# Performance work log

Hardware: AMD Instinct MI355X
Metric: run time of the kernel (lower is better)

The kernel has to match this reference:

```python
import jax, jax.numpy as jnp
import numpy as np

H = 1024   # hidden_dim
NH = 16    # num_heads
HD = H // NH  # head_dim = 64
B, S = 2, 2048
LN_EPS = 1e-5


def setup_inputs() -> dict:
    key = jax.random.key(0)
    ks = jax.random.split(key, 5)
    scale = 1.0 / np.sqrt(H)  # xavier-ish scale for stability
    return {
        "x": jax.random.normal(ks[0], (B, S, H), dtype=jnp.float32),
        "Wq": jax.random.normal(ks[1], (H, H), dtype=jnp.float32) * scale,
        "bq": jnp.zeros((H,), jnp.float32),
        "Wk": jax.random.normal(ks[2], (H, H), dtype=jnp.float32) * scale,
        "bk": jnp.zeros((H,), jnp.float32),
        "Wv": jax.random.normal(ks[3], (H, H), dtype=jnp.float32) * scale,
        "bv": jnp.zeros((H,), jnp.float32),
        "Wo": jax.random.normal(ks[4], (H, H), dtype=jnp.float32) * scale,
        "bo": jnp.zeros((H,), jnp.float32),
        "ln_gamma": jnp.ones((H,), jnp.float32),
        "ln_beta": jnp.zeros((H,), jnp.float32),
    }


def reference(x, Wq, bq, Wk, bk, Wv, bv, Wo, bo, ln_gamma, ln_beta):
    b, s, _ = x.shape
    # QKV projections, split heads: (b, nh, s, hd)
    def split_heads(t):
        return t.reshape(b, s, NH, HD).transpose(0, 2, 1, 3)
    Q = split_heads(x @ Wq + bq)
    K = split_heads(x @ Wk + bk)
    V = split_heads(x @ Wv + bv)
    # scaled dot-product with clamp (mask=None path)
    scores = jnp.einsum('bhqd,bhkd->bhqk', Q, K) / np.sqrt(HD).astype(np.float32)
    scores = jnp.clip(scores, -10000.0, 10000.0)
    attn = jax.nn.softmax(scores, axis=-1)
    # dropout is identity in eval mode
    ctx = jnp.einsum('bhqk,bhkd->bhqd', attn, V)
    ctx = ctx.transpose(0, 2, 1, 3).reshape(b, s, H)
    out = ctx @ Wo + bo
    # residual + LayerNorm
    y = out + x
    mu = jnp.mean(y, axis=-1, keepdims=True)
    var = jnp.mean(jnp.square(y - mu), axis=-1, keepdims=True)
    y = (y - mu) * jax.lax.rsqrt(var + LN_EPS)
    return y * ln_gamma + ln_beta
```

## Files before the change

### kernel.cpp

```cpp
#include <hip/hip_runtime.h>

typedef unsigned short u16;
typedef __attribute__((ext_vector_type(8))) short shortx8;
typedef __attribute__((ext_vector_type(4))) float floatx4;
typedef __attribute__((ext_vector_type(2))) float floatx2;
typedef __attribute__((ext_vector_type(2))) unsigned uintx2;
typedef __attribute__((ext_vector_type(4))) unsigned uintx4;

#define GLD16(gp, lp) __builtin_amdgcn_global_load_lds( \
    (__attribute__((address_space(1))) void*)(gp), \
    (__attribute__((address_space(3))) void*)(lp), 16, 0, 0)

#define BAR() __builtin_amdgcn_s_barrier()
#define LGKM0() do { asm volatile("s_waitcnt lgkmcnt(0)" ::: "memory"); \
                     __builtin_amdgcn_sched_barrier(0); } while (0)
#define VMCNT0() do { asm volatile("s_waitcnt vmcnt(0)" ::: "memory"); \
                      __builtin_amdgcn_sched_barrier(0); } while (0)

__device__ __forceinline__ u16 f2bf(float f) {
  union { float f; unsigned u; } v; v.f = f;
  unsigned r = v.u + 0x7FFFu + ((v.u >> 16) & 1u);
  return (u16)(r >> 16);
}

__device__ __forceinline__ unsigned pkbf(float a, float b) {
#if __has_builtin(__builtin_amdgcn_cvt_pk_bf16_f32)
  auto r = __builtin_amdgcn_cvt_pk_bf16_f32(a, b);
  return __builtin_bit_cast(unsigned, r);
#else
  union { float f; unsigned u; } x, y; x.f = a; y.f = b;
  return __builtin_amdgcn_perm(y.u + 0x8000u, x.u + 0x8000u, 0x07060302u);
#endif
}

__global__ __launch_bounds__(256) void prep_kernel(const float* __restrict__ x,
                                                   u16* __restrict__ xb,
                                                   const float* __restrict__ Wq,
                                                   const float* __restrict__ Wk,
                                                   const float* __restrict__ Wv,
                                                   const float* __restrict__ Wo,
                                                   u16* __restrict__ Wt) {
  __shared__ u16 tile[32][33];
  int bid = blockIdx.x;
  int tid = threadIdx.x;
  if (bid < 4096) {
    int i = bid * 256 + tid;
    float4 v = ((const float4*)x)[i];
    uintx2 o;
    o.x = pkbf(v.x, v.y);
    o.y = pkbf(v.z, v.w);
    ((uintx2*)xb)[i] = o;
  } else {
    int block = bid - 4096;
    int mat = block >> 10;
    int rem = block & 1023;
    const float* W = (mat == 0) ? Wq : (mat == 1) ? Wk : (mat == 2) ? Wv : Wo;
    u16* dst = Wt + (size_t)mat * 1024 * 1024;
    int n0 = (rem & 31) * 32, k0 = (rem >> 5) * 32;
    int tx = tid & 31, ty = tid >> 5;
    for (int i = 0; i < 4; ++i)
      tile[ty + i * 8][tx] = f2bf(W[(size_t)(k0 + ty + i * 8) * 1024 + n0 + tx]);
    __syncthreads();
    for (int i = 0; i < 4; ++i)
      dst[(size_t)(n0 + ty + i * 8) * 1024 + k0 + tx] = tile[tx][ty + i * 8];
  }
}

template <int MIB>
__device__ __forceinline__ void qkv_lda(const u16* Ah, int lrow, int lcol,
                                        shortx8 (&afr)[2][2]) {
#pragma unroll
  for (int j = 0; j < 2; ++j) {
    int rm = (MIB + j) * 16 + lcol;
#pragma unroll
    for (int kk = 0; kk < 2; ++kk)
      afr[j][kk] = *(const shortx8*)&Ah[rm * 64 + (((kk * 4 + lrow) ^ (rm & 7)) * 8)];
  }
}

template <int MIB>
__device__ __forceinline__ void qkv_mfma(floatx4 (&acc)[8][4],
                                         const shortx8 (&afr)[2][2],
                                         const shortx8 (&bfr)[4][2]) {
#pragma unroll
  for (int kk = 0; kk < 2; ++kk)
#pragma unroll
    for (int j = 0; j < 2; ++j)
#pragma unroll
      for (int ni = 0; ni < 4; ++ni)
        acc[MIB + j][ni] = __builtin_amdgcn_mfma_f32_16x16x32_bf16(
            afr[j][kk], bfr[ni][kk], acc[MIB + j][ni], 0, 0, 0);
}

__global__ __launch_bounds__(512, 2) void qkv_gemm(const u16* __restrict__ xb,
                                                   const u16* __restrict__ Wt,
                                                   const float* __restrict__ bq,
                                                   const float* __restrict__ bk,
                                                   const float* __restrict__ bv,
                                                   u16* __restrict__ Qh,
                                                   u16* __restrict__ Kh,
                                                   u16* __restrict__ Vth) {
  __shared__ u16 lds[65536];
  const int tid = threadIdx.x;
  const int wave = tid >> 6, lane = tid & 63;
  const int lrow = lane >> 4, lcol = lane & 15;
  const int wm = wave >> 2, wn = wave & 3;
  const int m0 = blockIdx.x * 256;
  const int nt = blockIdx.y;
  const int mat = nt >> 2;
  const int n0 = (nt & 3) * 256;
  const u16* Ag = xb;
  const u16* Bg = Wt + (size_t)mat * 1048576;

  const u16* sa[2][2];
  const u16* sb[2][2];
#pragma unroll
  for (int h = 0; h < 2; ++h)
#pragma unroll
    for (int l = 0; l < 2; ++l) {
      int g = (l * 8 + wave) * 64 + lane;
      int r = g >> 3, c = g & 7;
      int cc = (c ^ (r & 7)) * 8;
      sa[h][l] = Ag + (size_t)(m0 + h * 128 + r) * 1024 + cc;
      sb[h][l] = Bg + (size_t)(n0 + h * 128 + r) * 1024 + cc;
    }

  floatx4 acc[8][4];
#pragma unroll
  for (int mi = 0; mi < 8; ++mi)
#pragma unroll
    for (int ni = 0; ni < 4; ++ni)
      acc[mi][ni] = (floatx4){0.f, 0.f, 0.f, 0.f};

#pragma unroll
  for (int h = 0; h < 2; ++h)
#pragma unroll
    for (int l = 0; l < 2; ++l) {
      GLD16(sa[h][l], lds + h * 8192 + (l * 8 + wave) * 512);
      GLD16(sb[h][l], lds + 16384 + h * 8192 + (l * 8 + wave) * 512);
    }
  VMCNT0();
  BAR();

#pragma unroll 2
  for (int t = 0; t < 16; ++t) {
    const int rb = t & 1, wb = rb ^ 1;
    const u16* Ah = lds + rb * 32768 + wm * 8192;
    const u16* Bh = lds + rb * 32768 + 16384 + (wn >> 1) * 8192;
    u16* Aw = lds + wb * 32768;
    u16* Bw = lds + wb * 32768 + 16384;

    if (t < 15) {
      int k64 = (t + 1) * 64;
#pragma unroll
      for (int l = 0; l < 2; ++l) {
        GLD16(sa[0][l] + k64, Aw + (l * 8 + wave) * 512);
        GLD16(sa[1][l] + k64, Aw + 8192 + (l * 8 + wave) * 512);
      }
    }
    shortx8 bfr[4][2];
#pragma unroll
    for (int ni = 0; ni < 4; ++ni) {
      int rn = (wn & 1) * 64 + ni * 16 + lcol;
#pragma unroll
      for (int kk = 0; kk < 2; ++kk)
        bfr[ni][kk] = *(const shortx8*)&Bh[rn * 64 + (((kk * 4 + lrow) ^ (rn & 7)) * 8)];
    }
    {
      shortx8 afr[2][2];
      qkv_lda<0>(Ah, lrow, lcol, afr);
      BAR();
      LGKM0();
      __builtin_amdgcn_s_setprio(1);
      qkv_mfma<0>(acc, afr, bfr);
      __builtin_amdgcn_s_setprio(0);
      BAR();
    }
    if (t < 15) {
      int k64 = (t + 1) * 64;
#pragma unroll
      for (int l = 0; l < 2; ++l) {
        GLD16(sb[0][l] + k64, Bw + (l * 8 + wave) * 512);
        GLD16(sb[1][l] + k64, Bw + 8192 + (l * 8 + wave) * 512);
      }
    }
    {
      shortx8 afr[2][2];
      qkv_lda<2>(Ah, lrow, lcol, afr);
      BAR();
      LGKM0();
      __builtin_amdgcn_s_setprio(1);
      qkv_mfma<2>(acc, afr, bfr);
      __builtin_amdgcn_s_setprio(0);
      BAR();
    }
    {
      shortx8 afr[2][2];
      qkv_lda<4>(Ah, lrow, lcol, afr);
      BAR();
      LGKM0();
      __builtin_amdgcn_s_setprio(1);
      qkv_mfma<4>(acc, afr, bfr);
      __builtin_amdgcn_s_setprio(0);
      BAR();
    }
    {
      shortx8 afr[2][2];
      qkv_lda<6>(Ah, lrow, lcol, afr);
      BAR();
      LGKM0();
      __builtin_amdgcn_s_setprio(1);
      qkv_mfma<6>(acc, afr, bfr);
      __builtin_amdgcn_s_setprio(0);
      VMCNT0();
      BAR();
    }
  }

  const float* bias = (mat == 0) ? bq : (mat == 1) ? bk : bv;
  const float qscale = 0.18033688011f;

  if (mat < 2) {
    u16* dst = (mat == 0) ? Qh : Kh;
    float sc = (mat == 0) ? qscale : 1.0f;
#pragma unroll
    for (int mi = 0; mi < 8; ++mi) {
      int mb = wm * 128 + mi * 16 + lrow * 4;
#pragma unroll
      for (int ni = 0; ni < 4; ++ni) {
        int n = wn * 64 + ni * 16 + lcol;
        float bval = bias[n0 + n];
#pragma unroll
        for (int r = 0; r < 4; ++r) {
          int m = mb + r;
          lds[m * 256 + (((n >> 3) ^ (m & 31)) * 8) + (n & 7)] =
              f2bf((acc[mi][ni][r] + bval) * sc);
        }
      }
    }
    __syncthreads();
    int row = tid >> 1, half = tid & 1;
    int m = m0 + row;
    int bb = m >> 11, s = m & 2047;
#pragma unroll
    for (int i = 0; i < 16; ++i) {
      int cg = half * 16 + i;
      int pg = cg ^ (row & 31);
      shortx8 v = *(const shortx8*)&lds[row * 256 + pg * 8];
      int ng = n0 + cg * 8;
      int hh = ng >> 6, d = ng & 63;
      *(shortx8*)&dst[((size_t)(bb * 16 + hh) * 2048 + s) * 64 + d] = v;
    }
  } else {
#pragma unroll
    for (int mi = 0; mi < 8; ++mi) {
      int mbase = m0 + wm * 128 + mi * 16 + lrow * 4;
      int bb = mbase >> 11, s = mbase & 2047;
#pragma unroll
      for (int ni = 0; ni < 4; ++ni) {
        int n = n0 + wn * 64 + ni * 16 + lcol;
        float bval = bias[n];
        int hh = n >> 6, d = n & 63;
        uintx2 pk;
        pk.x = pkbf(acc[mi][ni][0] + bval, acc[mi][ni][1] + bval);
        pk.y = pkbf(acc[mi][ni][2] + bval, acc[mi][ni][3] + bval);
        *(uintx2*)&Vth[((size_t)(bb * 16 + hh) * 64 + d) * 2048 + s] = pk;
      }
    }
  }
}

__global__ __launch_bounds__(256, 2) void out_gemm(const u16* __restrict__ ctx,
                                                   const u16* __restrict__ Wot,
                                                   const float* __restrict__ bo,
                                                   float* __restrict__ aout) {
  __shared__ u16 lds[24576];
  const int tid = threadIdx.x;
  const int wave = tid >> 6, lane = tid & 63;
  const int lrow = lane >> 4, lcol = lane & 15;
  const int wm = wave >> 1, wn = wave & 1;
  const int m0 = blockIdx.x * 128;
  const int n0 = blockIdx.y * 64;

  const u16* sa[4];
  const u16* sb[2];
#pragma unroll
  for (int l = 0; l < 4; ++l) {
    int g = (l * 4 + wave) * 64 + lane;
    int r = g >> 3, c = g & 7;
    sa[l] = ctx + (size_t)(m0 + r) * 1024 + ((c ^ (r & 7)) * 8);
  }
#pragma unroll
  for (int l = 0; l < 2; ++l) {
    int g = (l * 4 + wave) * 64 + lane;
    int r = g >> 3, c = g & 7;
    sb[l] = Wot + (size_t)(n0 + r) * 1024 + ((c ^ (r & 7)) * 8);
  }

  floatx4 acc[4][2];
#pragma unroll
  for (int mi = 0; mi < 4; ++mi)
#pragma unroll
    for (int ni = 0; ni < 2; ++ni)
      acc[mi][ni] = (floatx4){0.f, 0.f, 0.f, 0.f};

#pragma unroll
  for (int l = 0; l < 4; ++l) GLD16(sa[l], lds + (l * 4 + wave) * 512);
#pragma unroll
  for (int l = 0; l < 2; ++l) GLD16(sb[l], lds + 8192 + (l * 4 + wave) * 512);
  VMCNT0();
  BAR();

#pragma unroll 2
  for (int t = 0; t < 16; ++t) {
    const int rb = t & 1, wb = rb ^ 1;
    const u16* Ab = lds + rb * 12288;
    const u16* Bb = lds + rb * 12288 + 8192;
    u16* Aw = lds + wb * 12288;
    u16* Bw = lds + wb * 12288 + 8192;
    const int k64 = (t + 1) * 64;

    if (t < 15) {
#pragma unroll
      for (int l = 0; l < 4; ++l) GLD16(sa[l] + k64, Aw + (l * 4 + wave) * 512);
    }
    shortx8 bfr[2][2];
#pragma unroll
    for (int ni = 0; ni < 2; ++ni) {
      int rn = wn * 32 + ni * 16 + lcol;
#pragma unroll
      for (int kk = 0; kk < 2; ++kk)
        bfr[ni][kk] = *(const shortx8*)&Bb[rn * 64 + (((kk * 4 + lrow) ^ (rn & 7)) * 8)];
    }
    {
      shortx8 afr[2][2];
#pragma unroll
      for (int j = 0; j < 2; ++j) {
        int rm = wm * 64 + j * 16 + lcol;
#pragma unroll
        for (int kk = 0; kk < 2; ++kk)
          afr[j][kk] = *(const shortx8*)&Ab[rm * 64 + (((kk * 4 + lrow) ^ (rm & 7)) * 8)];
      }
      BAR();
      LGKM0();
      __builtin_amdgcn_s_setprio(1);
#pragma unroll
      for (int kk = 0; kk < 2; ++kk)
#pragma unroll
        for (int j = 0; j < 2; ++j)
#pragma unroll
          for (int ni = 0; ni < 2; ++ni)
            acc[j][ni] = __builtin_amdgcn_mfma_f32_16x16x32_bf16(
                afr[j][kk], bfr[ni][kk], acc[j][ni], 0, 0, 0);
      __builtin_amdgcn_s_setprio(0);
      BAR();
    }
    if (t < 15) {
#pragma unroll
      for (int l = 0; l < 2; ++l) GLD16(sb[l] + k64, Bw + (l * 4 + wave) * 512);
    }
    {
      shortx8 afr[2][2];
#pragma unroll
      for (int j = 0; j < 2; ++j) {
        int rm = wm * 64 + (2 + j) * 16 + lcol;
#pragma unroll
        for (int kk = 0; kk < 2; ++kk)
          afr[j][kk] = *(const shortx8*)&Ab[rm * 64 + (((kk * 4 + lrow) ^ (rm & 7)) * 8)];
      }
      BAR();
      LGKM0();
      __builtin_amdgcn_s_setprio(1);
#pragma unroll
      for (int kk = 0; kk < 2; ++kk)
#pragma unroll
        for (int j = 0; j < 2; ++j)
#pragma unroll
          for (int ni = 0; ni < 2; ++ni)
            acc[2 + j][ni] = __builtin_amdgcn_mfma_f32_16x16x32_bf16(
                afr[j][kk], bfr[ni][kk], acc[2 + j][ni], 0, 0, 0);
      __builtin_amdgcn_s_setprio(0);
      VMCNT0();
      BAR();
    }
  }

#pragma unroll
  for (int mi = 0; mi < 4; ++mi) {
    int mbase = m0 + wm * 64 + mi * 16 + lrow * 4;
#pragma unroll
    for (int ni = 0; ni < 2; ++ni) {
      int n = n0 + wn * 32 + ni * 16 + lcol;
      float bval = bo[n];
#pragma unroll
      for (int r = 0; r < 4; ++r)
        aout[(size_t)(mbase + r) * 1024 + n] = acc[mi][ni][r] + bval;
    }
  }
}

__global__ __launch_bounds__(512) void attn_kernel(const u16* __restrict__ Qh,
                                                   const u16* __restrict__ Kh,
                                                   const u16* __restrict__ Vth,
                                                   u16* __restrict__ ctx) {
  __shared__ u16 QPs[128 * 64];
  __shared__ u16 Ks[2][64 * 64];
  __shared__ u16 Vs[2][64 * 64];

  int bh = blockIdx.x;
  int b = bh >> 4, h = bh & 15;
  int q0 = blockIdx.y * 128;
  int tid = threadIdx.x;
  int wave = tid >> 6, lane = tid & 63;
  int lrow = lane >> 4, lcol = lane & 15;

  const u16* Qg = Qh + ((size_t)bh * 2048 + q0) * 64;
  for (int l = 0; l < 2; ++l) {
    int g = (l * 8 + wave) * 64 + lane;
    int r = g >> 3, c = g & 7;
    GLD16(Qg + r * 64 + ((c ^ (r & 7)) * 8), QPs + (l * 8 + wave) * 512);
  }

  const u16* Kbase = Kh + (size_t)bh * 2048 * 64;
  const u16* Vbase = Vth + (size_t)bh * 64 * 2048;

  int g = wave * 64 + lane;
  int gr = g >> 3, gc = g & 7;
  int cc = (gc ^ (gr & 7)) * 8;
  const u16* kp = Kbase + (size_t)gr * 64 + cc;

  const u16* vp = Vbase + (size_t)gr * 2048 + gc * 8;
  int hh = gc >> 2, ct = gc & 3;
  int ua = 4 * (ct & 1) + (ct >> 1);
  int chunkA = hh * 4 + (ua >> 1);
  int offA = gr * 128 + ((chunkA ^ (gr & 7)) * 16) + (ua & 1) * 8;
  int offB = gr * 128 + (((chunkA + 1) ^ (gr & 7)) * 16) + (ua & 1) * 8;

  {
    float4 vreg = *(const float4*)vp;
    vp += 64;
    GLD16(kp, (u16*)Ks + wave * 512);
    kp += 4096;
    char* vb = (char*)Vs;
    *(floatx2*)(vb + offA) = (floatx2){vreg.x, vreg.y};
    *(floatx2*)(vb + offB) = (floatx2){vreg.z, vreg.w};
  }
  __syncthreads();

  shortx8 qf[2];
  for (int kk = 0; kk < 2; ++kk) {
    int row = wave * 16 + lcol;
    int grr = (kk * 4 + lrow) ^ (row & 7);
    qf[kk] = *(const shortx8*)&QPs[row * 64 + grr * 8];
  }

  const short one_bf = (short)0x3F80;
  const shortx8 ones8 = {one_bf, one_bf, one_bf, one_bf, one_bf, one_bf, one_bf, one_bf};

  floatx4 o[4];
  floatx4 lacc = (floatx4){0.f, 0.f, 0.f, 0.f};
  for (int dt = 0; dt < 4; ++dt) o[dt] = (floatx4){0.f, 0.f, 0.f, 0.f};

  for (int i = 0; i < 32; ++i) {
    int cur = i & 1;
    float4 vreg;
    if (i < 31) {
      vreg = *(const float4*)vp;
      vp += 64;
      GLD16(kp, (u16*)Ks + (cur ^ 1) * 4096 + wave * 512);
      kp += 4096;
    }

    floatx4 sc[4];
    for (int kt = 0; kt < 4; ++kt)
      sc[kt] = (floatx4){0.f, 0.f, 0.f, 0.f};
    __builtin_amdgcn_s_setprio(1);
    for (int kk = 0; kk < 2; ++kk) {
      for (int kt = 0; kt < 4; ++kt) {
        int row = kt * 16 + lcol;
        int grr = (kk * 4 + lrow) ^ (row & 7);
        shortx8 kf = *(const shortx8*)&Ks[cur][row * 64 + grr * 8];
        sc[kt] = __builtin_amdgcn_mfma_f32_16x16x32_bf16(kf, qf[kk], sc[kt], 0, 0, 0);
      }
    }
    __builtin_amdgcn_s_setprio(0);

    float p[4][4];
    for (int kt = 0; kt < 4; ++kt)
      for (int r = 0; r < 4; ++r)
        p[kt][r] = __builtin_amdgcn_exp2f(sc[kt][r]);
    shortx8 pf[2];
    for (int kk = 0; kk < 2; ++kk) {
      uintx4 w;
      w.x = pkbf(p[2 * kk][0], p[2 * kk][1]);
      w.y = pkbf(p[2 * kk][2], p[2 * kk][3]);
      w.z = pkbf(p[2 * kk + 1][0], p[2 * kk + 1][1]);
      w.w = pkbf(p[2 * kk + 1][2], p[2 * kk + 1][3]);
      pf[kk] = __builtin_bit_cast(shortx8, w);
    }

    if (i < 31) {
      char* vb = (char*)Vs + (cur ^ 1) * 8192;
      *(floatx2*)(vb + offA) = (floatx2){vreg.x, vreg.y};
      *(floatx2*)(vb + offB) = (floatx2){vreg.z, vreg.w};
    }

    __builtin_amdgcn_s_setprio(1);
    for (int kk = 0; kk < 2; ++kk) {
      lacc = __builtin_amdgcn_mfma_f32_16x16x32_bf16(ones8, pf[kk], lacc, 0, 0, 0);
      for (int dt = 0; dt < 4; ++dt) {
        int row = dt * 16 + lcol;
        int grr = (kk * 4 + lrow) ^ (row & 7);
        shortx8 vf = *(const shortx8*)&Vs[cur][row * 64 + grr * 8];
        o[dt] = __builtin_amdgcn_mfma_f32_16x16x32_bf16(vf, pf[kk], o[dt], 0, 0, 0);
      }
    }
    __builtin_amdgcn_s_setprio(0);
    __syncthreads();
  }

  {
    float inv = 1.0f / lacc[0];
    int s = q0 + wave * 16 + lcol;
    u16* dst = ctx + (size_t)(b * 2048 + s) * 1024 + h * 64 + lrow * 4;
    for (int dt = 0; dt < 4; ++dt) {
      uintx2 pk;
      pk.x = pkbf(o[dt][0] * inv, o[dt][1] * inv);
      pk.y = pkbf(o[dt][2] * inv, o[dt][3] * inv);
      *(uintx2*)(dst + dt * 16) = pk;
    }
  }
}

__global__ __launch_bounds__(256) void ln_kernel(const float* __restrict__ aout,
                                                 const float* __restrict__ x,
                                                 const float* __restrict__ gamma,
                                                 const float* __restrict__ beta,
                                                 float* __restrict__ out) {
  int row = blockIdx.x;
  int t = threadIdx.x;
  const float4* a4 = (const float4*)(aout + (size_t)row * 1024);
  const float4* x4 = (const float4*)(x + (size_t)row * 1024);
  float4 v = a4[t];
  float4 xv = x4[t];
  v.x += xv.x; v.y += xv.y; v.z += xv.z; v.w += xv.w;
  float s = v.x + v.y + v.z + v.w;
  float s2 = v.x * v.x + v.y * v.y + v.z * v.z + v.w * v.w;
  for (int off = 1; off < 64; off <<= 1) {
    s += __shfl_xor(s, off, 64);
    s2 += __shfl_xor(s2, off, 64);
  }
  __shared__ float red[8];
  int wave = t >> 6, lane = t & 63;
  if (lane == 0) { red[wave] = s; red[4 + wave] = s2; }
  __syncthreads();
  s = red[0] + red[1] + red[2] + red[3];
  s2 = red[4] + red[5] + red[6] + red[7];
  float mu = s * (1.0f / 1024.0f);
  float var = s2 * (1.0f / 1024.0f) - mu * mu;
  float rstd = rsqrtf(var + 1e-5f);
  float4 g = ((const float4*)gamma)[t];
  float4 be = ((const float4*)beta)[t];
  float4 y;
  y.x = (v.x - mu) * rstd * g.x + be.x;
  y.y = (v.y - mu) * rstd * g.y + be.y;
  y.z = (v.z - mu) * rstd * g.z + be.z;
  y.w = (v.w - mu) * rstd * g.w + be.w;
  ((float4*)(out + (size_t)row * 1024))[t] = y;
}

extern "C" void kernel_launch(void* const* d_in, const int* in_sizes, int n_in,
                              void* d_out, int out_size, void* d_ws, size_t ws_size,
                              hipStream_t stream) {
  const float* x     = (const float*)d_in[0];
  const float* Wq    = (const float*)d_in[1];
  const float* bq    = (const float*)d_in[2];
  const float* Wk    = (const float*)d_in[3];
  const float* bk    = (const float*)d_in[4];
  const float* Wv    = (const float*)d_in[5];
  const float* bv    = (const float*)d_in[6];
  const float* Wo    = (const float*)d_in[7];
  const float* bo    = (const float*)d_in[8];
  const float* gamma = (const float*)d_in[9];
  const float* beta  = (const float*)d_in[10];
  float* out = (float*)d_out;

  char* ws = (char*)d_ws;
  u16* xb   = (u16*)(ws);
  u16* Wt   = (u16*)(ws + ((size_t)8 << 20));
  u16* Qh   = (u16*)(ws + ((size_t)16 << 20));
  u16* Kh   = (u16*)(ws + ((size_t)24 << 20));
  u16* Vth  = (u16*)(ws + ((size_t)32 << 20));
  u16* ctx  = (u16*)(ws + ((size_t)40 << 20));
  float* aout = (float*)(ws + ((size_t)48 << 20));

  prep_kernel<<<8192, 256, 0, stream>>>(x, xb, Wq, Wk, Wv, Wo, Wt);
  qkv_gemm<<<dim3(16, 12), 512, 0, stream>>>(xb, Wt, bq, bk, bv, Qh, Kh, Vth);
  attn_kernel<<<dim3(32, 16), 512, 0, stream>>>(Qh, Kh, Vth, ctx);
  out_gemm<<<dim3(32, 16), 256, 0, stream>>>(ctx, Wt + (size_t)3 * 1024 * 1024, bo, aout);
  ln_kernel<<<4096, 256, 0, stream>>>(aout, x, gamma, beta, out);
}
```

Baseline: 193.0 us.

## Process two K/V tiles per attention loop iteration with doubled LDS buffers

The attention kernel now handles two 64-key tiles per iteration across 16 iterations, with four K and V LDS buffers. This halves the number of __syncthreads barriers and overlaps the second tile's QK MFMAs with the first tile's exp work. The cost is double the K/V shared memory (about 80KB per block), which may reduce occupancy, plus higher register pressure from two score sets.

```diff
diff --git a/kernel.cpp b/kernel.cpp
--- a/kernel.cpp
+++ b/kernel.cpp
@@ -404,8 +404,8 @@
                                                    const u16* __restrict__ Vth,
                                                    u16* __restrict__ ctx) {
   __shared__ u16 QPs[128 * 64];
-  __shared__ u16 Ks[2][64 * 64];
-  __shared__ u16 Vs[2][64 * 64];
+  __shared__ u16 Ks[4][64 * 64];
+  __shared__ u16 Vs[4][64 * 64];
 
   int bh = blockIdx.x;
   int b = bh >> 4, h = bh & 15;
@@ -437,13 +437,15 @@
   int offB = gr * 128 + (((chunkA + 1) ^ (gr & 7)) * 16) + (ua & 1) * 8;
 
   {
-    float4 vreg = *(const float4*)vp;
-    vp += 64;
-    GLD16(kp, (u16*)Ks + wave * 512);
-    kp += 4096;
+    float4 v0 = *(const float4*)vp; vp += 64;
+    float4 v1 = *(const float4*)vp; vp += 64;
+    GLD16(kp, (u16*)Ks + wave * 512);          kp += 4096;
+    GLD16(kp, (u16*)Ks + 4096 + wave * 512);   kp += 4096;
     char* vb = (char*)Vs;
-    *(floatx2*)(vb + offA) = (floatx2){vreg.x, vreg.y};
-    *(floatx2*)(vb + offB) = (floatx2){vreg.z, vreg.w};
+    *(floatx2*)(vb + offA) = (floatx2){v0.x, v0.y};
+    *(floatx2*)(vb + offB) = (floatx2){v0.z, v0.w};
+    *(floatx2*)(vb + 8192 + offA) = (floatx2){v1.x, v1.y};
+    *(floatx2*)(vb + 8192 + offB) = (floatx2){v1.z, v1.w};
   }
   __syncthreads();
 
@@ -461,58 +463,103 @@
   floatx4 lacc = (floatx4){0.f, 0.f, 0.f, 0.f};
   for (int dt = 0; dt < 4; ++dt) o[dt] = (floatx4){0.f, 0.f, 0.f, 0.f};
 
-  for (int i = 0; i < 32; ++i) {
-    int cur = i & 1;
-    float4 vreg;
-    if (i < 31) {
-      vreg = *(const float4*)vp;
-      vp += 64;
-      GLD16(kp, (u16*)Ks + (cur ^ 1) * 4096 + wave * 512);
-      kp += 4096;
-    }
-
-    floatx4 sc[4];
-    for (int kt = 0; kt < 4; ++kt)
-      sc[kt] = (floatx4){0.f, 0.f, 0.f, 0.f};
+#pragma unroll 1
+  for (int i = 0; i < 16; ++i) {
+    const int cur0 = (i & 1) * 2;
+    const int wbuf = ((i & 1) ^ 1) * 2;
+    float4 v0, v1;
+    if (i < 15) {
+      v0 = *(const float4*)vp; vp += 64;
+      v1 = *(const float4*)vp; vp += 64;
+      GLD16(kp, (u16*)Ks + wbuf * 4096 + wave * 512);        kp += 4096;
+      GLD16(kp, (u16*)Ks + (wbuf + 1) * 4096 + wave * 512);  kp += 4096;
+    }
+
+    floatx4 scA[4], scB[4];
+    for (int kt = 0; kt < 4; ++kt) {
+      scA[kt] = (floatx4){0.f, 0.f, 0.f, 0.f};
+      scB[kt] = (floatx4){0.f, 0.f, 0.f, 0.f};
+    }
     __builtin_amdgcn_s_setprio(1);
     for (int kk = 0; kk < 2; ++kk) {
       for (int kt = 0; kt < 4; ++kt) {
         int row = kt * 16 + lcol;
         int grr = (kk * 4 + lrow) ^ (row & 7);
-        shortx8 kf = *(const shortx8*)&Ks[cur][row * 64 + grr * 8];
-        sc[kt] = __builtin_amdgcn_mfma_f32_16x16x32_bf16(kf, qf[kk], sc[kt], 0, 0, 0);
+        shortx8 kf = *(const shortx8*)&Ks[cur0][row * 64 + grr * 8];
+        scA[kt] = __builtin_amdgcn_mfma_f32_16x16x32_bf16(kf, qf[kk], scA[kt], 0, 0, 0);
       }
     }
     __builtin_amdgcn_s_setprio(0);
 
-    float p[4][4];
-    for (int kt = 0; kt < 4; ++kt)
-      for (int r = 0; r < 4; ++r)
-        p[kt][r] = __builtin_amdgcn_exp2f(sc[kt][r]);
-    shortx8 pf[2];
-    for (int kk = 0; kk < 2; ++kk) {
-      uintx4 w;
-      w.x = pkbf(p[2 * kk][0], p[2 * kk][1]);
-      w.y = pkbf(p[2 * kk][2], p[2 * kk][3]);
-      w.z = pkbf(p[2 * kk + 1][0], p[2 * kk + 1][1]);
-      w.w = pkbf(p[2 * kk + 1][2], p[2 * kk + 1][3]);
-      pf[kk] = __builtin_bit_cast(shortx8, w);
-    }
-
-    if (i < 31) {
-      char* vb = (char*)Vs + (cur ^ 1) * 8192;
-      *(floatx2*)(vb + offA) = (floatx2){vreg.x, vreg.y};
-      *(floatx2*)(vb + offB) = (floatx2){vreg.z, vreg.w};
+    shortx8 pfA[2];
+    {
+      float p[4][4];
+      for (int kt = 0; kt < 4; ++kt)
+        for (int r = 0; r < 4; ++r)
+          p[kt][r] = __builtin_amdgcn_exp2f(scA[kt][r]);
+      for (int kk = 0; kk < 2; ++kk) {
+        uintx4 w;
+        w.x = pkbf(p[2 * kk][0], p[2 * kk][1]);
+        w.y = pkbf(p[2 * kk][2], p[2 * kk][3]);
+        w.z = pkbf(p[2 * kk + 1][0], p[2 * kk + 1][1]);
+        w.w = pkbf(p[2 * kk + 1][2], p[2 * kk + 1][3]);
+        pfA[kk] = __builtin_bit_cast(shortx8, w);
+      }
     }
 
     __builtin_amdgcn_s_setprio(1);
     for (int kk = 0; kk < 2; ++kk) {
-      lacc = __builtin_amdgcn_mfma_f32_16x16x32_bf16(ones8, pf[kk], lacc, 0, 0, 0);
+      for (int kt = 0; kt < 4; ++kt) {
+        int row = kt * 16 + lcol;
+        int grr = (kk * 4 + lrow) ^ (row & 7);
+        shortx8 kf = *(const shortx8*)&Ks[cur0 + 1][row * 64 + grr * 8];
+        scB[kt] = __builtin_amdgcn_mfma_f32_16x16x32_bf16(kf, qf[kk], scB[kt], 0, 0, 0);
+      }
+    }
+    __builtin_amdgcn_s_setprio(0);
+
+    shortx8 pfB[2];
+    {
+      float p[4][4];
+      for (int kt = 0; kt < 4; ++kt)
+        for (int r = 0; r < 4; ++r)
+          p[kt][r] = __builtin_amdgcn_exp2f(scB[kt][r]);
+      for (int kk = 0; kk < 2; ++kk) {
+        uintx4 w;
+        w.x = pkbf(p[2 * kk][0], p[2 * kk][1]);
+        w.y = pkbf(p[2 * kk][2], p[2 * kk][3]);
+        w.z = pkbf(p[2 * kk + 1][0], p[2 * kk + 1][1]);
+        w.w = pkbf(p[2 * kk + 1][2], p[2 * kk + 1][3]);
+        pfB[kk] = __builtin_bit_cast(shortx8, w);
+      }
+    }
+
+    if (i < 15) {
+      char* vb0 = (char*)Vs + wbuf * 8192;
+      char* vb1 = (char*)Vs + (wbuf + 1) * 8192;
+      *(floatx2*)(vb0 + offA) = (floatx2){v0.x, v0.y};
+      *(floatx2*)(vb0 + offB) = (floatx2){v0.z, v0.w};
+      *(floatx2*)(vb1 + offA) = (floatx2){v1.x, v1.y};
+      *(floatx2*)(vb1 + offB) = (floatx2){v1.z, v1.w};
+    }
+
+    __builtin_amdgcn_s_setprio(1);
+    for (int kk = 0; kk < 2; ++kk) {
+      lacc = __builtin_amdgcn_mfma_f32_16x16x32_bf16(ones8, pfA[kk], lacc, 0, 0, 0);
       for (int dt = 0; dt < 4; ++dt) {
         int row = dt * 16 + lcol;
         int grr = (kk * 4 + lrow) ^ (row & 7);
-        shortx8 vf = *(const shortx8*)&Vs[cur][row * 64 + grr * 8];
-        o[dt] = __builtin_amdgcn_mfma_f32_16x16x32_bf16(vf, pf[kk], o[dt], 0, 0, 0);
+        shortx8 vf = *(const shortx8*)&Vs[cur0][row * 64 + grr * 8];
+        o[dt] = __builtin_amdgcn_mfma_f32_16x16x32_bf16(vf, pfA[kk], o[dt], 0, 0, 0);
+      }
+    }
+    for (int kk = 0; kk < 2; ++kk) {
+      lacc = __builtin_amdgcn_mfma_f32_16x16x32_bf16(ones8, pfB[kk], lacc, 0, 0, 0);
+      for (int dt = 0; dt < 4; ++dt) {
+        int row = dt * 16 + lcol;
+        int grr = (kk * 4 + lrow) ^ (row & 7);
+        shortx8 vf = *(const shortx8*)&Vs[cur0 + 1][row * 64 + grr * 8];
+        o[dt] = __builtin_amdgcn_mfma_f32_16x16x32_bf16(vf, pfB[kk], o[dt], 0, 0, 0);
       }
     }
     __builtin_amdgcn_s_setprio(0);
```

Result: slower. 197.3 us (+2.2%).
